# Kernel optimization log

Hardware: AMD Instinct MI355X
Metric: run time of the kernel (lower is better)

The kernel has to match this reference:

```python
import jax, jax.numpy as jnp
import numpy as np

GROUPS = 32
EPS = 1e-5


def setup_inputs() -> dict:
    key = jax.random.key(0)
    ks = jax.random.split(key, 4)
    B, C, H, W = 32, 512, 32, 32
    x = jax.random.normal(ks[0], (B, C, H, W), dtype=jnp.float32)
    gn_gamma = jnp.ones((C,), jnp.float32)
    gn_beta = jnp.zeros((C,), jnp.float32)
    qkv_w = jax.random.normal(ks[1], (3 * C, C), dtype=jnp.float32) * 0.02
    qkv_b = jnp.zeros((3 * C,), jnp.float32)
    proj_w = jax.random.normal(ks[2], (C, C), dtype=jnp.float32) * 0.02
    proj_b = jnp.zeros((C,), jnp.float32)
    return {"x": x, "gn_gamma": gn_gamma, "gn_beta": gn_beta,
            "qkv_w": qkv_w, "qkv_b": qkv_b, "proj_w": proj_w, "proj_b": proj_b}


def group_norm(x, gamma, beta):
    B, C, H, W = x.shape
    xr = x.reshape(B, GROUPS, C // GROUPS, H, W)
    mean = xr.mean(axis=(2, 3, 4), keepdims=True)
    var = xr.var(axis=(2, 3, 4), keepdims=True)
    xn = ((xr - mean) * jax.lax.rsqrt(var + EPS)).reshape(B, C, H, W)
    return xn * gamma[None, :, None, None] + beta[None, :, None, None]


def reference(x, gn_gamma, gn_beta, qkv_w, qkv_b, proj_w, proj_b):
    B, C, H, W = x.shape
    h_in = group_norm(x, gn_gamma, gn_beta)
    # 1x1 conv == per-pixel matmul over channels
    qkv = jnp.einsum('oc,bchw->bohw', qkv_w, h_in) + qkv_b[None, :, None, None]
    q, k, v = jnp.split(qkv, 3, axis=1)
    scale = 1.0 / jnp.sqrt(jnp.sqrt(jnp.float32(C)))  # 1/sqrt(sqrt(C)), applied to q and k
    attn = jnp.einsum('bchw,bcij->bhwij', q * scale, k * scale)  # [B,H,W,H,W]
    attn = jax.nn.softmax(attn, axis=-1)  # faithful: softmax over last axis (j) only
    h = jnp.einsum('bhwij,bcij->bchw', attn, v)
    h = jnp.einsum('oc,bchw->bohw', proj_w, h) + proj_b[None, :, None, None]
    return x + h
```

## Files before the change

### kernel.cpp

```cpp
#include <hip/hip_runtime.h>

typedef __attribute__((ext_vector_type(8))) short short8;
typedef __attribute__((ext_vector_type(4))) float f32x4;

__device__ __forceinline__ float b2f(unsigned short u) {
  union { unsigned u32; float f; } x; x.u32 = ((unsigned)u) << 16; return x.f;
}
__device__ __forceinline__ unsigned short f2bf(float f) {
  union { float f; unsigned u; } x; x.f = f;
  unsigned r = x.u + 0x7fffu + ((x.u >> 16) & 1u);
  return (unsigned short)(r >> 16);
}
__device__ __forceinline__ void async_load16(const void* g, void* l) {
  __builtin_amdgcn_global_load_lds(
      (__attribute__((address_space(1))) void*)(void*)(g),
      (__attribute__((address_space(3))) void*)(l), 16, 0, 0);
}

__global__ __launch_bounds__(256) void cvt2_k(
    const float* __restrict__ a, unsigned short* __restrict__ oa, int n4a,
    const float* __restrict__ bsrc, unsigned short* __restrict__ ob, int n4b) {
  int i = blockIdx.x * 256 + threadIdx.x;
  const float* src; unsigned short* dst; int idx;
  if (i < n4a) { src = a; dst = oa; idx = i; }
  else if (i < n4a + n4b) { src = bsrc; dst = ob; idx = i - n4a; }
  else return;
  float4 v = ((const float4*)src)[idx];
  unsigned short o[4] __attribute__((aligned(8)));
  o[0] = f2bf(v.x); o[1] = f2bf(v.y); o[2] = f2bf(v.z); o[3] = f2bf(v.w);
  ((int2*)dst)[idx] = *(int2*)o;
}

__global__ __launch_bounds__(256) void groupnorm_k(
    const float* __restrict__ x, const float* __restrict__ gamma,
    const float* __restrict__ beta, unsigned short* __restrict__ hin) {
  const int b = blockIdx.x >> 5, g = blockIdx.x & 31;
  const float* xb = x + ((unsigned long long)b * 512ull + (unsigned long long)g * 16ull) * 1024ull;
  const int t = threadIdx.x;
  float4 xr[16];
  float s = 0.f, ss = 0.f;
#pragma unroll
  for (int c = 0; c < 16; ++c) {
    xr[c] = *(const float4*)(xb + c * 1024 + t * 4);
    s += xr[c].x + xr[c].y + xr[c].z + xr[c].w;
    ss += xr[c].x * xr[c].x + xr[c].y * xr[c].y + xr[c].z * xr[c].z + xr[c].w * xr[c].w;
  }
#pragma unroll
  for (int o = 32; o; o >>= 1) { s += __shfl_down(s, o); ss += __shfl_down(ss, o); }
  __shared__ float sred[8];
  if ((t & 63) == 0) { sred[t >> 6] = s; sred[4 + (t >> 6)] = ss; }
  __syncthreads();
  s = sred[0] + sred[1] + sred[2] + sred[3];
  ss = sred[4] + sred[5] + sred[6] + sred[7];
  const float mean = s * (1.f / 16384.f);
  const float rstd = rsqrtf(ss * (1.f / 16384.f) - mean * mean + 1e-5f);
  float ga[16], be[16];
#pragma unroll
  for (int c = 0; c < 16; ++c) {
    float gg = gamma[g * 16 + c] * rstd;
    ga[c] = gg;
    be[c] = beta[g * 16 + c] - mean * gg;
  }
#pragma unroll
  for (int p4 = 0; p4 < 4; ++p4) {
    unsigned short ov[16] __attribute__((aligned(16)));
#pragma unroll
    for (int c = 0; c < 16; ++c)
      ov[c] = f2bf(((const float*)&xr[c])[p4] * ga[c] + be[c]);
    unsigned short* dst = hin + ((unsigned long long)b * 1024ull + t * 4 + p4) * 512ull + g * 16;
    *(int4*)dst = *(int4*)ov;
    *(int4*)(dst + 8) = *(int4*)(ov + 8);
  }
}

template <int MODE>
__global__ __launch_bounds__(512, 2) void gemm_k(
    const unsigned short* __restrict__ A, unsigned long long sA, int lda,
    const unsigned short* __restrict__ B, unsigned long long sB, int ldb,
    const float* __restrict__ bias, const float* __restrict__ xres,
    unsigned short* __restrict__ out0, unsigned short* __restrict__ out1,
    unsigned short* __restrict__ out2, float* __restrict__ fout,
    float scale, int K) {
  __shared__ unsigned short smem[65536];
  const int tid = threadIdx.x;
  const int wave = tid >> 6, lane = tid & 63;

  int n_t, m_t, b;
  if (MODE == 0) {
    const int L = blockIdx.x;
    const int r8 = L & 7, q = L >> 3;
    n_t = q % 6;
    const int mb = (q / 6) * 8 + r8;
    m_t = mb & 3;
    b = mb >> 2;
  } else if (MODE == 1) {
    const int L = blockIdx.x;
    const int slice = L & 7, t = L >> 3;
    b = slice * 4 + (t >> 4);
    const int rem = t & 15;
    m_t = rem >> 2;
    n_t = rem & 3;
  } else if (MODE == 2) {
    const int L = blockIdx.x;
    const int slice = L & 7, t = L >> 3;
    b = slice * 4 + (t >> 3);
    const int rem = t & 7;
    m_t = rem >> 1;
    n_t = rem & 1;
  } else {
    n_t = blockIdx.x; m_t = blockIdx.y; b = blockIdx.z;
  }
  const int m0 = m_t * 256, n0 = n_t * 256;
  const int wm = (wave & 1) * 128, wn = (wave >> 1) * 64;
  const unsigned short* Ab = A + (unsigned long long)b * sA + (unsigned long long)m0 * lda;
  const unsigned short* Bb = B + (unsigned long long)b * sB + (unsigned long long)n0 * ldb;

  f32x4 acc[8][4];
#pragma unroll
  for (int i = 0; i < 8; ++i)
#pragma unroll
    for (int j = 0; j < 4; ++j)
#pragma unroll
      for (int r = 0; r < 4; ++r) acc[i][j][r] = 0.f;

  const int lrow = lane & 15;
  const int lk = lane >> 4;
  const int sr = lane >> 3;
  const int pc = (((lane & 7) ^ sr) << 3);
  const int r7 = lrow & 7;
  const int arow = wave * 32;

  auto STAGE = [&](int kt, int buf) {
    unsigned short* As_ = smem + buf * 32768;
    unsigned short* Bs_ = As_ + 16384;
#pragma unroll
    for (int c = 0; c < 4; ++c) {
      async_load16(Ab + kt + (unsigned long long)(arow + c * 8 + sr) * lda + pc,
                   (void*)(As_ + (arow + c * 8) * 64));
      async_load16(Bb + kt + (unsigned long long)(arow + c * 8 + sr) * ldb + pc,
                   (void*)(Bs_ + (arow + c * 8) * 64));
    }
  };
  auto COMPUTE = [&](int buf) {
    const unsigned short* As = smem + buf * 32768;
    const unsigned short* Bs = As + 16384;
#pragma unroll
    for (int ks = 0; ks < 2; ++ks) {
      const int ko = (((ks << 2) + lk) ^ r7) << 3;
      short8 af[8], bfr[4];
#pragma unroll
      for (int i = 0; i < 8; ++i)
        af[i] = *(const short8*)(As + (wm + i * 16 + lrow) * 64 + ko);
#pragma unroll
      for (int i = 0; i < 4; ++i)
        bfr[i] = *(const short8*)(Bs + (wn + i * 16 + lrow) * 64 + ko);
      __builtin_amdgcn_s_setprio(1);
#pragma unroll
      for (int mi = 0; mi < 8; ++mi)
#pragma unroll
        for (int ni = 0; ni < 4; ++ni)
          acc[mi][ni] = __builtin_amdgcn_mfma_f32_16x16x32_bf16(af[mi], bfr[ni], acc[mi][ni], 0, 0, 0);
      __builtin_amdgcn_s_setprio(0);
    }
  };

  const int nt = K >> 6;
  STAGE(0, 0);
  STAGE(64, 1);
  for (int t = 0; t < nt - 1; ++t) {
    asm volatile("s_waitcnt vmcnt(8)" ::: "memory");
    __builtin_amdgcn_s_barrier();
    COMPUTE(t & 1);
    __builtin_amdgcn_sched_barrier(0);
    __builtin_amdgcn_s_barrier();
    if (t + 2 < nt) STAGE((t + 2) << 6, t & 1);
  }
  asm volatile("s_waitcnt vmcnt(0)" ::: "memory");
  __builtin_amdgcn_s_barrier();
  COMPUTE((nt - 1) & 1);

  const int r0 = lk * 4;
  const int cn = lrow;

  if (MODE == 0) {
    const int which = n0 >> 9;
#pragma unroll
    for (int ni = 0; ni < 4; ++ni) {
      const int o = n0 + wn + ni * 16 + cn;
      const float bi = bias[o];
      const int oin = o & 511;
      if (which < 2) {
        unsigned short* dst = (which == 0 ? out0 : out1) + (unsigned long long)b * 524288ull;
#pragma unroll
        for (int mi = 0; mi < 8; ++mi) {
          const int pbase = m0 + wm + mi * 16 + r0;
#pragma unroll
          for (int r = 0; r < 4; ++r)
            dst[(unsigned long long)(pbase + r) * 512ull + oin] = f2bf((acc[mi][ni][r] + bi) * scale);
        }
      } else {
        unsigned short* dst = out2 + (unsigned long long)b * 524288ull + (unsigned long long)oin * 1024ull;
#pragma unroll
        for (int mi = 0; mi < 8; ++mi) {
          const int pbase = m0 + wm + mi * 16 + r0;
          unsigned short h4[4] __attribute__((aligned(8)));
#pragma unroll
          for (int r = 0; r < 4; ++r) h4[r] = f2bf(acc[mi][ni][r] + bi);
          *(int2*)(dst + pbase) = *(int2*)h4;
        }
      }
    }
  } else if (MODE == 1) {
#pragma unroll
    for (int mi = 0; mi < 8; ++mi)
#pragma unroll
      for (int ni = 0; ni < 4; ++ni)
#pragma unroll
        for (int r = 0; r < 4; ++r) acc[mi][ni][r] = __expf(acc[mi][ni][r]);
    float inv[4][4];
#pragma unroll
    for (int ni = 0; ni < 4; ++ni)
#pragma unroll
      for (int cp = 0; cp < 4; ++cp) {
        float s8 = 0.f;
#pragma unroll
        for (int mm = 0; mm < 2; ++mm)
#pragma unroll
          for (int r = 0; r < 4; ++r) s8 += acc[cp * 2 + mm][ni][r];
        s8 += __shfl_xor(s8, 16);
        s8 += __shfl_xor(s8, 32);
        inv[ni][cp] = 1.f / s8;
      }
    unsigned short* Pt = smem;
    unsigned short* dst = out0 + (unsigned long long)b * 1048576ull;
#pragma unroll
    for (int half = 0; half < 2; ++half) {
      __syncthreads();
      if ((wn >> 7) == half) {
        const int lbase = wn - half * 128;
#pragma unroll
        for (int mi = 0; mi < 8; ++mi)
#pragma unroll
          for (int ni = 0; ni < 4; ++ni) {
            unsigned short p4[4] __attribute__((aligned(8)));
#pragma unroll
            for (int r = 0; r < 4; ++r) p4[r] = f2bf(acc[mi][ni][r] * inv[ni][mi >> 1]);
            const int li = lbase + ni * 16 + cn;
            const int lj = wm + mi * 16 + r0;
            *(int2*)(Pt + li * 264 + lj) = *(int2*)p4;
          }
      }
      __syncthreads();
#pragma unroll
      for (int it = 0; it < 8; ++it) {
        const int row = it * 16 + (tid >> 5);
        const int col = (tid & 31) * 8;
        int4 v = *(const int4*)(Pt + row * 264 + col);
        *(int4*)(dst + (unsigned long long)(n0 + half * 128 + row) * 1024ull + m0 + col) = v;
      }
    }
  } else if (MODE == 2) {
    unsigned short* dst = out0 + (unsigned long long)b * 524288ull;
#pragma unroll
    for (int mi = 0; mi < 8; ++mi) {
      const int ib = m0 + wm + mi * 16 + r0;
#pragma unroll
      for (int ni = 0; ni < 4; ++ni) {
        const int c = n0 + wn + ni * 16 + cn;
#pragma unroll
        for (int r = 0; r < 4; ++r)
          dst[(unsigned long long)(ib + r) * 512ull + c] = f2bf(acc[mi][ni][r]);
      }
    }
  } else {
    float* dst = fout + (unsigned long long)b * 524288ull;
    const float* xr = xres + (unsigned long long)b * 524288ull;
#pragma unroll
    for (int mi = 0; mi < 8; ++mi) {
      const int ob = m0 + wm + mi * 16 + r0;
#pragma unroll
      for (int r = 0; r < 4; ++r) {
        const int o = ob + r;
        const float bi = bias[o];
#pragma unroll
        for (int ni = 0; ni < 4; ++ni) {
          const int p = n0 + wn + ni * 16 + cn;
          const unsigned long long idx = (unsigned long long)o * 1024ull + p;
          dst[idx] = acc[mi][ni][r] + bi + xr[idx];
        }
      }
    }
  }
}

extern "C" void kernel_launch(void* const* d_in, const int* in_sizes, int n_in,
                              void* d_out, int out_size, void* d_ws, size_t ws_size,
                              hipStream_t stream) {
  const float* x     = (const float*)d_in[0];
  const float* gamma = (const float*)d_in[1];
  const float* beta  = (const float*)d_in[2];
  const float* qkvw  = (const float*)d_in[3];
  const float* qkvb  = (const float*)d_in[4];
  const float* projw = (const float*)d_in[5];
  const float* projb = (const float*)d_in[6];
  float* out = (float*)d_out;
  char* ws = (char*)d_ws;

  unsigned short* Hin = (unsigned short*)(ws);
  unsigned short* Q   = (unsigned short*)(ws + 1ull * 33554432ull);
  unsigned short* Kb  = (unsigned short*)(ws + 2ull * 33554432ull);
  unsigned short* V   = (unsigned short*)(ws + 3ull * 33554432ull);
  unsigned short* S   = (unsigned short*)(ws + 4ull * 33554432ull);
  unsigned short* Wq  = (unsigned short*)(ws + 6ull * 33554432ull);
  unsigned short* Wp  = (unsigned short*)(ws + 6ull * 33554432ull + 2ull * 1048576ull);
  unsigned short* H   = Hin;

  const float SCALE = 0.21022410381342864f;
  const float* nzf = nullptr;
  unsigned short* nzo = nullptr;
  float* nzfo = nullptr;

  hipLaunchKernelGGL(cvt2_k, dim3(1024), dim3(256), 0, stream, qkvw, Wq, 196608, projw, Wp, 65536);
  hipLaunchKernelGGL(groupnorm_k, dim3(1024), dim3(256), 0, stream, x, gamma, beta, Hin);
  hipLaunchKernelGGL((gemm_k<0>), dim3(768), dim3(512), 0, stream,
                     Hin, 524288ull, 512, Wq, 0ull, 512, qkvb, nzf, Q, Kb, V, nzfo, SCALE, 512);
  hipLaunchKernelGGL((gemm_k<1>), dim3(512), dim3(512), 0, stream,
                     Kb, 524288ull, 512, Q, 524288ull, 512, nzf, nzf, S, nzo, nzo, nzfo, 0.f, 512);
  hipLaunchKernelGGL((gemm_k<2>), dim3(256), dim3(512), 0, stream,
                     S, 1048576ull, 1024, V, 524288ull, 1024, nzf, nzf, H, nzo, nzo, nzfo, 0.f, 1024);
  hipLaunchKernelGGL((gemm_k<3>), dim3(4, 2, 32), dim3(512), 0, stream,
                     Wp, 0ull, 512, H, 524288ull, 512, projb, x, nzo, nzo, nzo, out, 0.f, 512);
}
```

Baseline: 341.0 us.

## Interleave quarter-tile async staging with half-step MFMA phases in GEMM main loop

Replaces the two-stage prefetch, in which a whole 64-wide K tile was issued after the compute, with a finer schedule. The next tile's A/B loads are split into four quarters, each issued between MFMA phases with extra barriers. A-fragment registers are halved (4 instead of 8) and the compute is split into four 16-MFMA blocks. This aims to spread global-to-LDS traffic across the compute and reduce register pressure. The cost is more barriers per iteration and a prefetch distance of one tile instead of two, which may expose more memory latency.

```diff
diff --git a/kernel.cpp b/kernel.cpp
--- a/kernel.cpp
+++ b/kernel.cpp
@@ -128,56 +128,78 @@
   const int sr = lane >> 3;
   const int pc = (((lane & 7) ^ sr) << 3);
   const int r7 = lrow & 7;
-  const int arow = wave * 32;
-
-  auto STAGE = [&](int kt, int buf) {
-    unsigned short* As_ = smem + buf * 32768;
-    unsigned short* Bs_ = As_ + 16384;
-#pragma unroll
-    for (int c = 0; c < 4; ++c) {
-      async_load16(Ab + kt + (unsigned long long)(arow + c * 8 + sr) * lda + pc,
-                   (void*)(As_ + (arow + c * 8) * 64));
-      async_load16(Bb + kt + (unsigned long long)(arow + c * 8 + sr) * ldb + pc,
-                   (void*)(Bs_ + (arow + c * 8) * 64));
-    }
+
+  auto STAGE_HALF = [&](int kt, int buf, int hh) {
+    const unsigned short* gsrc = (hh < 2) ? Ab : Bb;
+    const int ld = (hh < 2) ? lda : ldb;
+    const int hrow = (hh & 1) * 128 + wave * 16;
+    unsigned short* ldst = smem + buf * 32768 + ((hh < 2) ? 0 : 16384) + hrow * 64;
+#pragma unroll
+    for (int c = 0; c < 2; ++c)
+      async_load16(gsrc + kt + (unsigned long long)(hrow + c * 8 + sr) * ld + pc,
+                   (void*)(ldst + c * 8 * 64));
   };
-  auto COMPUTE = [&](int buf) {
-    const unsigned short* As = smem + buf * 32768;
+
+  short8 af[4], bfr[4];
+  auto LOAD_A = [&](const unsigned short* As, int h, int ks) {
+    const int ko = (((ks << 2) + lk) ^ r7) << 3;
+#pragma unroll
+    for (int i = 0; i < 4; ++i)
+      af[i] = *(const short8*)(As + (wm + (h * 4 + i) * 16 + lrow) * 64 + ko);
+  };
+  auto LOAD_B = [&](const unsigned short* Bs, int ks) {
+    const int ko = (((ks << 2) + lk) ^ r7) << 3;
+#pragma unroll
+    for (int i = 0; i < 4; ++i)
+      bfr[i] = *(const short8*)(Bs + (wn + i * 16 + lrow) * 64 + ko);
+  };
+  auto MFMA16 = [&](int h) {
+    __builtin_amdgcn_s_setprio(1);
+#pragma unroll
+    for (int mi = 0; mi < 4; ++mi)
+#pragma unroll
+      for (int ni = 0; ni < 4; ++ni)
+        acc[h * 4 + mi][ni] =
+            __builtin_amdgcn_mfma_f32_16x16x32_bf16(af[mi], bfr[ni], acc[h * 4 + mi][ni], 0, 0, 0);
+    __builtin_amdgcn_s_setprio(0);
+  };
+
+  const int nt = K >> 6;
+#pragma unroll
+  for (int hh = 0; hh < 4; ++hh) STAGE_HALF(0, 0, hh);
+
+  for (int t = 0; t < nt; ++t) {
+    const unsigned short* As = smem + (t & 1) * 32768;
     const unsigned short* Bs = As + 16384;
-#pragma unroll
-    for (int ks = 0; ks < 2; ++ks) {
-      const int ko = (((ks << 2) + lk) ^ r7) << 3;
-      short8 af[8], bfr[4];
-#pragma unroll
-      for (int i = 0; i < 8; ++i)
-        af[i] = *(const short8*)(As + (wm + i * 16 + lrow) * 64 + ko);
-#pragma unroll
-      for (int i = 0; i < 4; ++i)
-        bfr[i] = *(const short8*)(Bs + (wn + i * 16 + lrow) * 64 + ko);
-      __builtin_amdgcn_s_setprio(1);
-#pragma unroll
-      for (int mi = 0; mi < 8; ++mi)
-#pragma unroll
-        for (int ni = 0; ni < 4; ++ni)
-          acc[mi][ni] = __builtin_amdgcn_mfma_f32_16x16x32_bf16(af[mi], bfr[ni], acc[mi][ni], 0, 0, 0);
-      __builtin_amdgcn_s_setprio(0);
-    }
-  };
-
-  const int nt = K >> 6;
-  STAGE(0, 0);
-  STAGE(64, 1);
-  for (int t = 0; t < nt - 1; ++t) {
-    asm volatile("s_waitcnt vmcnt(8)" ::: "memory");
-    __builtin_amdgcn_s_barrier();
-    COMPUTE(t & 1);
-    __builtin_amdgcn_sched_barrier(0);
-    __builtin_amdgcn_s_barrier();
-    if (t + 2 < nt) STAGE((t + 2) << 6, t & 1);
-  }
-  asm volatile("s_waitcnt vmcnt(0)" ::: "memory");
-  __builtin_amdgcn_s_barrier();
-  COMPUTE((nt - 1) & 1);
+    const int kn = (t + 1) << 6;
+    const int nb = (t + 1) & 1;
+    const bool more = (t + 1 < nt);
+    if (more) {
+      STAGE_HALF(kn, nb, 0);
+      asm volatile("s_waitcnt vmcnt(2)" ::: "memory");
+    } else {
+      asm volatile("s_waitcnt vmcnt(0)" ::: "memory");
+    }
+    __builtin_amdgcn_s_barrier();
+    LOAD_A(As, 0, 0); LOAD_B(Bs, 0);
+    MFMA16(0);
+    __builtin_amdgcn_s_barrier();
+    if (more) STAGE_HALF(kn, nb, 1);
+    LOAD_A(As, 1, 0);
+    __builtin_amdgcn_s_barrier();
+    MFMA16(1);
+    __builtin_amdgcn_s_barrier();
+    if (more) STAGE_HALF(kn, nb, 2);
+    LOAD_A(As, 1, 1); LOAD_B(Bs, 1);
+    __builtin_amdgcn_s_barrier();
+    MFMA16(1);
+    __builtin_amdgcn_s_barrier();
+    if (more) STAGE_HALF(kn, nb, 3);
+    LOAD_A(As, 0, 1);
+    __builtin_amdgcn_s_barrier();
+    MFMA16(0);
+    __builtin_amdgcn_s_barrier();
+  }
 
   const int r0 = lk * 4;
   const int cn = lrow;
```

Measured after the change: 344.7 us. Within noise of the previous version (+1.1%).
